# Kernel tuning notes

Hardware: AMD Instinct MI355X
Metric: run time of the kernel (lower is better)

The kernel has to match this reference:

```python
import jax, jax.numpy as jnp
import numpy as np
from jax import lax

V, D, P, C = 151936, 1024, 64, 28
B, S = 1, 1024
EPS = 1.1920929e-07  # torch.finfo(float32).eps, used by nn.RMSNorm(eps=None)


def setup_inputs() -> dict:
    key = jax.random.key(0)
    ks = jax.random.split(key, 10)
    return {
        "tokens": jax.random.randint(ks[0], (B, S), 0, V),
        "embed_table": jax.random.normal(ks[1], (V, D), jnp.float32) * 0.02,
        "plane_proj_w": jax.random.normal(ks[2], (C, 2 * P, D), jnp.float32) * (1.0 / np.sqrt(D)),
        "back_proj_w": jax.random.normal(ks[3], (C, D, 2 * P), jnp.float32) * 0.02,
        "base_angles": jax.random.normal(ks[4], (C, P), jnp.float32) * 0.1,
        "angle_gen_w": jax.random.normal(ks[5], (P, D), jnp.float32) * 0.01,
        "scales": jnp.ones((C, D), jnp.float32),
        "shifts": jnp.zeros((C, D), jnp.float32),
        "norm_w": jnp.ones((C, D), jnp.float32),
        "decay_param": jnp.float32(0.9),
        "gate_w": jax.random.normal(ks[6], (D, D), jnp.float32) * 0.02,
        "out_norm_w": jnp.ones((D,), jnp.float32),
        "lm_head_w": jax.random.normal(ks[7], (V, D), jnp.float32) * 0.02,
    }


def _rms_norm(v, w):
    return v * lax.rsqrt(jnp.mean(v * v, axis=-1, keepdims=True) + EPS) * w


def _causal_mix(x, decay_param, gate_w):
    # state_t = d*state_{t-1} + (1-d)*x_t, causal EMA over sequence
    d = jax.nn.sigmoid(decay_param)
    def step(s, xt):
        s = d * s + (1.0 - d) * xt
        return s, s
    _, ys = lax.scan(step, jnp.zeros(x.shape[::2], x.dtype)[0:0].sum(0) + jnp.zeros((x.shape[0], x.shape[2]), x.dtype), jnp.swapaxes(x, 0, 1))
    causal = jnp.swapaxes(ys, 0, 1)  # [B,S,D]
    return x + causal @ gate_w.T


def reference(tokens, embed_table, plane_proj_w, back_proj_w, base_angles,
              angle_gen_w, scales, shifts, norm_w, decay_param, gate_w,
              out_norm_w, lm_head_w):
    x = embed_table[tokens].astype(jnp.float32)  # [B,S,D]
    n_cycles = scales.shape[0]
    for i in range(n_cycles):
        # input-dependent angle offset (detached in the original)
        extra = x.mean(axis=1) @ angle_gen_w.T          # [B,P]
        angles = base_angles[i] + lax.stop_gradient(extra.mean(axis=0)) * 0.1
        if i % 4 == 0:
            x = _causal_mix(x, decay_param, gate_w)
        # learned-plane rotation
        proj = x @ plane_proj_w[i].T                     # [B,S,2P]
        n = proj.shape[-1] // 2
        a, b = proj[..., :n], proj[..., n:]
        ca, sa = jnp.cos(angles), jnp.sin(angles)
        rot = jnp.concatenate([a * ca - b * sa, a * sa + b * ca], axis=-1)
        x_rot = x + rot @ back_proj_w[i].T
        x_act = jax.nn.silu(x_rot * scales[i] + shifts[i])
        x = x + _rms_norm(x_act - x, norm_w[i])
    x = _rms_norm(x, out_norm_w)
    return x @ lm_head_w.T  # [B,S,V]
```

## Files before the change

### kernel.cpp

```cpp
#include <hip/hip_runtime.h>

typedef __attribute__((ext_vector_type(4))) float f32x4;
typedef __attribute__((ext_vector_type(8))) short bf16x8;
typedef unsigned short u16;
typedef unsigned int u32;
typedef __attribute__((ext_vector_type(4))) unsigned short u16x4;

#define EPS 1.1920929e-07f
#define S 1024
#define D 1024
#define NV 151936
#define NCYC 28
#define SMEM_BYTES 49152

__device__ __forceinline__ u16 f2bf(float f) {
  u32 u = __float_as_uint(f);
  return (u16)((u + 0x7fffu + ((u >> 16) & 1u)) >> 16);
}
__device__ __forceinline__ float bf2f(u16 h) {
  return __uint_as_float((u32)h << 16);
}
struct bfpair { u16 h, l; };
__device__ __forceinline__ bfpair split_bf(float v) {
  bfpair r;
  r.h = f2bf(v);
  r.l = f2bf(v - bf2f(r.h));
  return r;
}

__device__ __forceinline__ void gl16(const void* g, void* s) {
  __builtin_amdgcn_global_load_lds((const __attribute__((address_space(1))) u32*)g,
                                   (__attribute__((address_space(3))) u32*)s, 16, 0, 0);
}

__device__ __forceinline__ float block_sum256(float v, float* sbuf) {
  #pragma unroll
  for (int off = 32; off; off >>= 1) v += __shfl_down(v, off);
  int lane = threadIdx.x & 63, w = threadIdx.x >> 6;
  __syncthreads();
  if (lane == 0) sbuf[w] = v;
  __syncthreads();
  return sbuf[0] + sbuf[1] + sbuf[2] + sbuf[3];
}

__device__ void cvt2_range(const float* __restrict__ src, u16* __restrict__ dh,
                           u16* __restrict__ dl, size_t n4, int blkbase, int nblk) {
  for (size_t i = (size_t)(blockIdx.x - blkbase) * 256 + threadIdx.x; i < n4;
       i += (size_t)nblk * 256) {
    f32x4 v = ((const f32x4*)src)[i];
    u16x4 oh, ol;
    #pragma unroll
    for (int e = 0; e < 4; ++e) { bfpair p = split_bf(v[e]); oh[e] = p.h; ol[e] = p.l; }
    ((u16x4*)dh)[i] = oh;
    ((u16x4*)dl)[i] = ol;
  }
}

__device__ void side_cvt(const float* __restrict__ src, u16* __restrict__ dst,
                         int chunk, int blkbase) {
  const size_t n4 = (size_t)NV * D / 4;
  const size_t per = (n4 + (size_t)(NCYC * 3) - 1) / (size_t)(NCYC * 3);
  size_t lo = (size_t)chunk * per;
  size_t hi = lo + per;
  if (hi > n4) hi = n4;
  const size_t nb = (size_t)(gridDim.x - blkbase);
  for (size_t i = lo + (size_t)(blockIdx.x - blkbase) * 256 + threadIdx.x; i < hi;
       i += nb * 256) {
    f32x4 v = ((const f32x4*)src)[i];
    u16x4 o;
    #pragma unroll
    for (int e = 0; e < 4; ++e) o[e] = f2bf(v[e]);
    ((u16x4*)dst)[i] = o;
  }
}


__device__ void gather_phase(const int* tokens, const float* embed,
                             float* x, u16* xh, u16* xl, float* cp) {
  const int t = threadIdx.x;
  f32x4 creg = 0.f;
  for (int rr = 0; rr < 4; ++rr) {
    int s = blockIdx.x * 4 + rr;
    int tok = tokens[s];
    f32x4 v = ((const f32x4*)(embed + (size_t)tok * D))[t];
    u16x4 oh, ol;
    #pragma unroll
    for (int e = 0; e < 4; ++e) { bfpair p = split_bf(v[e]); oh[e] = p.h; ol[e] = p.l; }
    ((f32x4*)(x + (size_t)s * D))[t] = v;
    ((u16x4*)(xh + (size_t)s * D))[t] = oh;
    ((u16x4*)(xl + (size_t)s * D))[t] = ol;
    creg += v;
  }
  *(f32x4*)(cp + (size_t)blockIdx.x * D + t * 4) = creg;
}

template <bool CADD>
__device__ void gemm64_dbuf(char* smem, const u16* Ah_, const u16* Al_,
                            const u16* Bh_, const u16* Bl_, int K,
                            float* xout, u16* xho, u16* xlo, float* Cout) {
  const int t = threadIdx.x;
  u16* Ash = (u16*)smem;
  u16* Asl = Ash + 8192;
  u16* Bsh = Asl + 8192;
  u16* Bsl = Bsh + 8192;
  const int wave = t >> 6, lane = t & 63;
  const int fr = lane & 15, kb = lane >> 4;
  const int sr = t >> 3, skc = (t & 7) << 3;
  const int sswz = skc ^ ((sr & 7) << 3);
  const int m0 = (blockIdx.x >> 4) * 64, n0 = (blockIdx.x & 15) * 64;
  f32x4 acc[4];
  #pragma unroll
  for (int j = 0; j < 4; ++j) acc[j] = 0.f;

  auto stage = [&](int buf, int k0) {
    #pragma unroll
    for (int it = 0; it < 2; ++it) {
      int r = it * 32 + sr;
      size_t ga = (size_t)(m0 + r) * K + k0 + sswz;
      size_t gb = (size_t)(n0 + r) * K + k0 + sswz;
      int so = buf * 4096 + r * 64 + skc;
      gl16(Ah_ + ga, Ash + so);
      gl16(Al_ + ga, Asl + so);
      gl16(Bh_ + gb, Bsh + so);
      gl16(Bl_ + gb, Bsl + so);
    }
  };
  const int nt = K >> 6;
  stage(0, 0);
  __syncthreads();
  for (int kt = 0; kt < nt; ++kt) {
    const int cur = kt & 1;
    if (kt + 1 < nt) stage(cur ^ 1, (kt + 1) << 6);
    const int co = cur * 4096;
    #pragma unroll
    for (int ks = 0; ks < 2; ++ks) {
      const int cphys = (ks * 32 + kb * 8) ^ ((fr & 7) << 3);
      int oa = co + (wave * 16 + fr) * 64 + cphys;
      bf16x8 ah = *(const bf16x8*)&Ash[oa];
      bf16x8 al = *(const bf16x8*)&Asl[oa];
      #pragma unroll
      for (int j = 0; j < 4; ++j) {
        int ob = co + (j * 16 + fr) * 64 + cphys;
        bf16x8 bh = *(const bf16x8*)&Bsh[ob];
        bf16x8 bl = *(const bf16x8*)&Bsl[ob];
        acc[j] = __builtin_amdgcn_mfma_f32_16x16x32_bf16(ah, bh, acc[j], 0, 0, 0);
        acc[j] = __builtin_amdgcn_mfma_f32_16x16x32_bf16(ah, bl, acc[j], 0, 0, 0);
        acc[j] = __builtin_amdgcn_mfma_f32_16x16x32_bf16(al, bh, acc[j], 0, 0, 0);
      }
    }
    __syncthreads();
  }
  #pragma unroll
  for (int j = 0; j < 4; ++j)
    #pragma unroll
    for (int rg = 0; rg < 4; ++rg) {
      int m = m0 + wave * 16 + kb * 4 + rg;
      int n = n0 + j * 16 + fr;
      if (CADD) {
        float v = xout[(size_t)m * D + n] + acc[j][rg];
        xout[(size_t)m * D + n] = v;
        bfpair p = split_bf(v);
        xho[(size_t)m * D + n] = p.h;
        xlo[(size_t)m * D + n] = p.l;
      } else {
        Cout[(size_t)m * D + n] = acc[j][rg];
      }
    }
}

__device__ void causal_phase(char* smem, const float* x, u16* Rh, u16* Rl,
                             float dec, int G) {
  const int t = threadIdx.x;
  for (int tile = blockIdx.x; tile < 256; tile += G) {
    int s0 = (tile >> 4) * 64, d0 = (tile & 15) * 64;
    float (*tl)[64] = (float(*)[64])smem;
    for (int idx = t; idx < 159 * 64; idx += 256) {
      int rr = idx >> 6, c = idx & 63;
      int gs = s0 - 95 + rr;
      tl[rr][c] = (gs >= 0) ? x[(size_t)gs * D + d0 + c] : 0.f;
    }
    __syncthreads();
    int c = t & 63, r0 = t >> 6;
    for (int rr = r0; rr < 64; rr += 4) {
      float acc = 0.f, w = 1.f - dec;
      int base = rr + 95;
      #pragma unroll 8
      for (int j = 0; j < 96; ++j) { acc += w * tl[base - j][c]; w *= dec; }
      bfpair p = split_bf(acc);
      Rh[(size_t)(s0 + rr) * D + d0 + c] = p.h;
      Rl[(size_t)(s0 + rr) * D + d0 + c] = p.l;
    }
    __syncthreads();
  }
}

__device__ void proj_phase(char* smem, const u16* xh, const u16* xl,
                           const u16* Bh_, const u16* Bl_, float* pacc) {
  const int t = threadIdx.x;
  const int mt = blockIdx.x & 15, kq = blockIdx.x >> 4;
  const int m0 = mt * 64;
  const int k0 = kq * 64;
  u16* Ash = (u16*)smem;
  u16* Asl = Ash + 4096;
  u16* Bsh = Asl + 4096;
  u16* Bsl = Bsh + 8192;
  const int wave = t >> 6, lane = t & 63;
  const int fr = lane & 15, kb = lane >> 4;
  const int sr = t >> 3, skc = (t & 7) << 3;
  const int sswz = skc ^ ((sr & 7) << 3);
  f32x4 acc[8];
  #pragma unroll
  for (int j = 0; j < 8; ++j) acc[j] = 0.f;

  #pragma unroll
  for (int it = 0; it < 2; ++it) {
    int r = it * 32 + sr;
    size_t ga = (size_t)(m0 + r) * D + k0 + sswz;
    gl16(xh + ga, Ash + r * 64 + skc);
    gl16(xl + ga, Asl + r * 64 + skc);
  }
  #pragma unroll
  for (int it = 0; it < 4; ++it) {
    int r = it * 32 + sr;
    size_t gb = (size_t)r * D + k0 + sswz;
    gl16(Bh_ + gb, Bsh + r * 64 + skc);
    gl16(Bl_ + gb, Bsl + r * 64 + skc);
  }
  __syncthreads();
  #pragma unroll
  for (int ks = 0; ks < 2; ++ks) {
    const int cphys = (ks * 32 + kb * 8) ^ ((fr & 7) << 3);
    int oa = (wave * 16 + fr) * 64 + cphys;
    bf16x8 ah = *(const bf16x8*)&Ash[oa];
    bf16x8 al = *(const bf16x8*)&Asl[oa];
    #pragma unroll
    for (int j = 0; j < 8; ++j) {
      int ob = (j * 16 + fr) * 64 + cphys;
      bf16x8 bh = *(const bf16x8*)&Bsh[ob];
      bf16x8 bl = *(const bf16x8*)&Bsl[ob];
      acc[j] = __builtin_amdgcn_mfma_f32_16x16x32_bf16(ah, bh, acc[j], 0, 0, 0);
      acc[j] = __builtin_amdgcn_mfma_f32_16x16x32_bf16(ah, bl, acc[j], 0, 0, 0);
      acc[j] = __builtin_amdgcn_mfma_f32_16x16x32_bf16(al, bh, acc[j], 0, 0, 0);
    }
  }
  float* pb = pacc + (size_t)blockIdx.x * 64 * 128;
  #pragma unroll
  for (int j = 0; j < 8; ++j)
    #pragma unroll
    for (int rg = 0; rg < 4; ++rg) {
      int ml = wave * 16 + kb * 4 + rg;
      pb[ml * 128 + j * 16 + fr] = acc[j][rg];
    }
}

__device__ void angles_all(float* colsum, const float* cp, const float* agw,
                           const float* bang_i, float* trig) {
  const int t = threadIdx.x;
  f32x4 acc = 0.f;
  for (int b = 0; b < 256; ++b)
    acc += *(const f32x4*)(cp + (size_t)b * D + t * 4);
  *(f32x4*)&colsum[t * 4] = acc;
  __syncthreads();
  const int wave = t >> 6, lane = t & 63;
  for (int pp = 0; pp < 16; ++pp) {
    int p = wave * 16 + pp;
    float sum = 0.f;
    #pragma unroll
    for (int q = 0; q < 16; ++q) {
      int d = lane + q * 64;
      sum += colsum[d] * agw[p * D + d];
    }
    #pragma unroll
    for (int off = 32; off; off >>= 1) sum += __shfl_down(sum, off);
    if (lane == 0) {
      float ang = bang_i[p] + 0.1f * (sum * (1.f / (float)S));
      trig[p] = cosf(ang);
      trig[64 + p] = sinf(ang);
    }
  }
}

__device__ void epilogue_phase(float* sbuf, float* x, u16* xh, u16* xl,
                               const float* Rf, const float* scale,
                               const float* shift, const float* nw, float* cp) {
  const int t = threadIdx.x;
  f32x4 sc = *(const f32x4*)(scale + t * 4);
  f32x4 sh = *(const f32x4*)(shift + t * 4);
  f32x4 nwv = *(const f32x4*)(nw + t * 4);
  f32x4 creg = 0.f;
  for (int rr = 0; rr < 4; ++rr) {
    int s = blockIdx.x * 4 + rr;
    f32x4 xv = *(const f32x4*)(x + (size_t)s * D + t * 4);
    f32x4 rv = *(const f32x4*)(Rf + (size_t)s * D + t * 4);
    float y[4], ss = 0.f;
    #pragma unroll
    for (int c = 0; c < 4; ++c) {
      float xr = xv[c] + rv[c];
      float tt = xr * sc[c] + sh[c];
      float act = tt / (1.f + expf(-tt));
      y[c] = act - xv[c];
      ss += y[c] * y[c];
    }
    float total = block_sum256(ss, sbuf);
    float inv = rsqrtf(total * (1.f / (float)D) + EPS);
    f32x4 o;
    u16x4 oh, ol;
    #pragma unroll
    for (int c = 0; c < 4; ++c) {
      o[c] = xv[c] + y[c] * inv * nwv[c];
      bfpair p = split_bf(o[c]);
      oh[c] = p.h;
      ol[c] = p.l;
      creg[c] += o[c];
    }
    *(f32x4*)(x + (size_t)s * D + t * 4) = o;
    *(u16x4*)(xh + (size_t)s * D + t * 4) = oh;
    *(u16x4*)(xl + (size_t)s * D + t * 4) = ol;
  }
  *(f32x4*)(cp + (size_t)blockIdx.x * D + t * 4) = creg;
}

__device__ void outnorm_phase(float* sbuf, const float* x, const float* w, u16* xn) {
  const int t = threadIdx.x;
  for (int rr = 0; rr < 4; ++rr) {
    int s = blockIdx.x * 4 + rr;
    f32x4 xv = *(const f32x4*)(x + (size_t)s * D + t * 4);
    float total = block_sum256(xv[0]*xv[0] + xv[1]*xv[1] + xv[2]*xv[2] + xv[3]*xv[3], sbuf);
    float inv = rsqrtf(total * (1.f / (float)D) + EPS);
    f32x4 wv = *(const f32x4*)(w + t * 4);
    u16x4 o;
    #pragma unroll
    for (int c = 0; c < 4; ++c) o[c] = f2bf(xv[c] * inv * wv[c]);
    *(u16x4*)(xn + (size_t)s * D + t * 4) = o;
  }
}

__global__ __launch_bounds__(256) void fb_gather(const int* tokens, const float* embed,
                                                 float* x, u16* xh, u16* xl, float* cp,
                                                 const float* gatew, u16* gh, u16* gl,
                                                 const float* Wp, u16* Wph, u16* Wpl,
                                                 const float* Wb, u16* Wbh, u16* Wbl) {
  if (blockIdx.x < 256) {
    gather_phase(tokens, embed, x, xh, xl, cp);
  } else if (blockIdx.x < 384) {
    cvt2_range(gatew, gh, gl, (size_t)D * D / 4, 256, 128);
  } else if (blockIdx.x < 576) {
    cvt2_range(Wp, Wph, Wpl, (size_t)NCYC * 128 * D / 4, 384, 192);
  } else {
    cvt2_range(Wb, Wbh, Wbl, (size_t)NCYC * 128 * D / 4, 576, 192);
  }
}
__global__ __launch_bounds__(256) void fb_causal(const float* x, u16* Rh, u16* Rl,
                                                 const float* decay) {
  __shared__ __align__(16) char sm[40704];
  causal_phase(sm, x, Rh, Rl, 1.f / (1.f + expf(-decay[0])), gridDim.x);
}
__global__ __launch_bounds__(256) void fb_gate(const u16* Rh, const u16* Rl,
                                               const u16* gh, const u16* gl,
                                               float* x, u16* xh, u16* xl) {
  __shared__ __align__(16) char sm[65536];
  gemm64_dbuf<true>(sm, Rh, Rl, gh, gl, 1024, x, xh, xl, nullptr);
}
__global__ __launch_bounds__(256) void fb_proj(const u16* xh, const u16* xl,
                                               const u16* Wph, const u16* Wpl,
                                               const float* cp, const float* agw,
                                               const float* bang_i,
                                               float* pacc, float* trig,
                                               const float* lmw, u16* lm_bf, int chunk) {
  __shared__ __align__(16) char sm[SMEM_BYTES];
  if (blockIdx.x < 256) proj_phase(sm, xh, xl, Wph, Wpl, pacc);
  else if (blockIdx.x == 256) angles_all((float*)sm, cp, agw, bang_i, trig);
  else side_cvt(lmw, lm_bf, chunk, 257);
}

__global__ __launch_bounds__(256) void fb_back(const float* __restrict__ pacc,
                                               const float* __restrict__ trig,
                                               const u16* __restrict__ Bh_,
                                               const u16* __restrict__ Bl_,
                                               float* __restrict__ Rf,
                                               const float* lmw, u16* lm_bf, int chunk) {
  __shared__ u16 Ash[64 * 128];
  __shared__ u16 Asl[64 * 128];
  __shared__ u16 Bsh[64 * 64];
  __shared__ u16 Bsl[64 * 64];
  if (blockIdx.x >= 256) { side_cvt(lmw, lm_bf, chunk, 256); return; }
  const int t = threadIdx.x;
  const int tile = blockIdx.x;
  const int mt = tile >> 4;
  const int m0 = mt * 64, n0 = (tile & 15) * 64;
  const int wave = t >> 6, lane = t & 63;
  const int fr = lane & 15, kb = lane >> 4;
  const int sr = t >> 3, skc = (t & 7) << 3;
  const int sswz = skc ^ ((sr & 7) << 3);

  #pragma unroll
  for (int ri = 0; ri < 2; ++ri) {
    int r = ri * 32 + sr;
    int pdst = skc ^ ((r & 7) << 3);
    f32x4 a0 = 0.f, a1 = 0.f, b0 = 0.f, b1 = 0.f;
    #pragma unroll
    for (int kq = 0; kq < 16; ++kq) {
      const float* pk = pacc + ((size_t)(kq * 16 + mt) * 64 + r) * 128;
      a0 += *(const f32x4*)(pk + skc);
      a1 += *(const f32x4*)(pk + skc + 4);
      b0 += *(const f32x4*)(pk + 64 + skc);
      b1 += *(const f32x4*)(pk + 64 + skc + 4);
    }
    #pragma unroll
    for (int kh = 0; kh < 2; ++kh) {
      u16 hbuf[8], lbuf[8];
      #pragma unroll
      for (int j = 0; j < 8; ++j) {
        float av = (j < 4) ? a0[j & 3] : a1[j & 3];
        float bv = (j < 4) ? b0[j & 3] : b1[j & 3];
        float ca = trig[skc + j], sa = trig[64 + skc + j];
        float v = (kh == 0) ? (av * ca - bv * sa) : (av * sa + bv * ca);
        bfpair p = split_bf(v);
        hbuf[j] = p.h;
        lbuf[j] = p.l;
      }
      int so = r * 128 + kh * 64 + pdst;
      *(bf16x8*)&Ash[so] = *(bf16x8*)hbuf;
      *(bf16x8*)&Asl[so] = *(bf16x8*)lbuf;
    }
  }
  __syncthreads();

  f32x4 acc[4];
  #pragma unroll
  for (int j = 0; j < 4; ++j) acc[j] = 0.f;

  for (int kt = 0; kt < 2; ++kt) {
    int k0 = kt * 64;
    #pragma unroll
    for (int it = 0; it < 2; ++it) {
      int r = it * 32 + sr;
      size_t gb = (size_t)(n0 + r) * 128 + k0 + sswz;
      gl16(Bh_ + gb, Bsh + r * 64 + skc);
      gl16(Bl_ + gb, Bsl + r * 64 + skc);
    }
    __syncthreads();
    #pragma unroll
    for (int ks = 0; ks < 2; ++ks) {
      const int w = (ks * 32 + kb * 8) ^ ((fr & 7) << 3);
      int oa = (wave * 16 + fr) * 128 + k0 + w;
      bf16x8 ah = *(const bf16x8*)&Ash[oa];
      bf16x8 al = *(const bf16x8*)&Asl[oa];
      #pragma unroll
      for (int j = 0; j < 4; ++j) {
        int ob = (j * 16 + fr) * 64 + w;
        bf16x8 bh = *(const bf16x8*)&Bsh[ob];
        bf16x8 bl = *(const bf16x8*)&Bsl[ob];
        acc[j] = __builtin_amdgcn_mfma_f32_16x16x32_bf16(ah, bh, acc[j], 0, 0, 0);
        acc[j] = __builtin_amdgcn_mfma_f32_16x16x32_bf16(ah, bl, acc[j], 0, 0, 0);
        acc[j] = __builtin_amdgcn_mfma_f32_16x16x32_bf16(al, bh, acc[j], 0, 0, 0);
      }
    }
    __syncthreads();
  }
  #pragma unroll
  for (int j = 0; j < 4; ++j)
    #pragma unroll
    for (int rg = 0; rg < 4; ++rg) {
      int m = m0 + wave * 16 + kb * 4 + rg;
      int n = n0 + j * 16 + fr;
      Rf[(size_t)m * D + n] = acc[j][rg];
    }
}

__global__ __launch_bounds__(256) void fb_epi(float* x, u16* xh, u16* xl, const float* Rf,
                                              const float* scale, const float* shift,
                                              const float* nw, float* cp,
                                              const float* lmw, u16* lm_bf, int chunk) {
  __shared__ float sbuf[4];
  if (blockIdx.x < 256) epilogue_phase(sbuf, x, xh, xl, Rf, scale, shift, nw, cp);
  else side_cvt(lmw, lm_bf, chunk, 256);
}
__global__ __launch_bounds__(256) void fb_outnorm(const float* x, const float* w, u16* xn) {
  __shared__ float sbuf[4];
  outnorm_phase(sbuf, x, w, xn);
}

template <bool PRECONV>
__global__ __launch_bounds__(256) void k_lm(const u16* __restrict__ A,
                                            const void* __restrict__ Wsrc,
                                            float* __restrict__ out) {
  __shared__ u16 As[128 * 64];
  __shared__ u16 Bs[128 * 64];
  const int bid = blockIdx.x;
  const int lid = (bid & 7) * 1187 + (bid >> 3);
  const int m0 = (lid & 7) * 128;
  const int n0 = (lid >> 3) * 128;
  const int t = threadIdx.x;
  const int wave = t >> 6, lane = t & 63;
  const int wm = (wave >> 1) * 64, wn = (wave & 1) * 64;
  const int fr = lane & 15, kb = lane >> 4;
  const int sr = t >> 3, skc = (t & 7) << 3;
  const int sswz = skc ^ ((sr & 7) << 3);
  const u16* Wb16 = (const u16*)Wsrc;
  const float* Wf = (const float*)Wsrc;
  f32x4 acc[4][4];
  #pragma unroll
  for (int i = 0; i < 4; ++i)
    #pragma unroll
    for (int j = 0; j < 4; ++j) acc[i][j] = 0.f;

  for (int k0 = 0; k0 < D; k0 += 64) {
    #pragma unroll
    for (int it = 0; it < 4; ++it) {
      int r = it * 32 + sr;
      gl16(A + (size_t)(m0 + r) * D + k0 + sswz, As + r * 64 + skc);
    }
    if (PRECONV) {
      #pragma unroll
      for (int it = 0; it < 4; ++it) {
        int r = it * 32 + sr;
        gl16(Wb16 + (size_t)(n0 + r) * D + k0 + sswz, Bs + r * 64 + skc);
      }
    } else {
      #pragma unroll
      for (int it = 0; it < 4; ++it) {
        int r = it * 32 + sr;
        const float* src = Wf + (size_t)(n0 + r) * D + k0 + sswz;
        f32x4 v0 = *(const f32x4*)src;
        f32x4 v1 = *(const f32x4*)(src + 4);
        u16 h[8];
        #pragma unroll
        for (int e = 0; e < 4; ++e) { h[e] = f2bf(v0[e]); h[e + 4] = f2bf(v1[e]); }
        *(bf16x8*)&Bs[r * 64 + skc] = *(bf16x8*)h;
      }
    }
    __syncthreads();
    #pragma unroll
    for (int ks = 0; ks < 2; ++ks) {
      const int cphys = (ks * 32 + kb * 8) ^ ((fr & 7) << 3);
      bf16x8 a[4], b[4];
      #pragma unroll
      for (int i = 0; i < 4; ++i) a[i] = *(const bf16x8*)&As[(wm + i * 16 + fr) * 64 + cphys];
      #pragma unroll
      for (int j = 0; j < 4; ++j) b[j] = *(const bf16x8*)&Bs[(wn + j * 16 + fr) * 64 + cphys];
      #pragma unroll
      for (int i = 0; i < 4; ++i)
        #pragma unroll
        for (int j = 0; j < 4; ++j)
          acc[i][j] = __builtin_amdgcn_mfma_f32_16x16x32_bf16(a[i], b[j], acc[i][j], 0, 0, 0);
    }
    __syncthreads();
  }
  #pragma unroll
  for (int i = 0; i < 4; ++i)
    #pragma unroll
    for (int j = 0; j < 4; ++j)
      #pragma unroll
      for (int rg = 0; rg < 4; ++rg) {
        int m = m0 + wm + i * 16 + kb * 4 + rg;
        int n = n0 + wn + j * 16 + fr;
        out[(size_t)m * NV + n] = acc[i][j][rg];
      }
}

extern "C" void kernel_launch(void* const* d_in, const int* in_sizes, int n_in,
                              void* d_out, int out_size, void* d_ws, size_t ws_size,
                              hipStream_t stream) {
  const int* tokens = (const int*)d_in[0];
  const float* embed = (const float*)d_in[1];
  const float* Wp = (const float*)d_in[2];
  const float* Wb = (const float*)d_in[3];
  const float* bang = (const float*)d_in[4];
  const float* agw = (const float*)d_in[5];
  const float* scales = (const float*)d_in[6];
  const float* shifts = (const float*)d_in[7];
  const float* normw = (const float*)d_in[8];
  const float* decay = (const float*)d_in[9];
  const float* gatew = (const float*)d_in[10];
  const float* onorm = (const float*)d_in[11];
  const float* lmw = (const float*)d_in[12];
  float* out = (float*)d_out;

  char* ws = (char*)d_ws;
  const size_t MB = 1u << 20;
  float* x = (float*)ws;
  u16* xh = (u16*)(ws + 4 * MB);
  u16* xl = (u16*)(ws + 6 * MB);
  float* Rf = (float*)(ws + 8 * MB);
  u16* Rh = (u16*)(ws + 12 * MB);
  u16* Rl = (u16*)(ws + 14 * MB);
  float* trig = (float*)(ws + 16 * MB);
  float* cp = (float*)(ws + 17 * MB);
  u16* xn = (u16*)(ws + 20 * MB);
  u16* gate_h = (u16*)(ws + 22 * MB);
  u16* gate_l = (u16*)(ws + 24 * MB);
  u16* Wp_h = (u16*)(ws + 26 * MB);
  u16* Wp_l = (u16*)(ws + 33 * MB);
  u16* Wb_h = (u16*)(ws + 40 * MB);
  u16* Wb_l = (u16*)(ws + 47 * MB);
  float* pacc = (float*)(ws + 54 * MB);
  u16* lm_bf = (u16*)(ws + 62 * MB);

  const size_t lm_elems = (size_t)NV * D;
  bool preconv = ws_size >= 62 * MB + lm_elems * 2;
  const float* side_src = preconv ? lmw : nullptr;
  u16* side_dst = preconv ? lm_bf : nullptr;
  const int gproj = preconv ? 385 : 257;
  const int gside = preconv ? 384 : 256;

  fb_gather<<<768, 256, 0, stream>>>(tokens, embed, x, xh, xl, cp,
                                     gatew, gate_h, gate_l,
                                     Wp, Wp_h, Wp_l, Wb, Wb_h, Wb_l);
  for (int i = 0; i < NCYC; ++i) {
    const u16* Wph = Wp_h + (size_t)i * 128 * D;
    const u16* Wpl = Wp_l + (size_t)i * 128 * D;
    const u16* Wbh = Wb_h + (size_t)i * 128 * D;
    const u16* Wbl = Wb_l + (size_t)i * 128 * D;
    if ((i & 3) == 0) {
      fb_causal<<<256, 256, 0, stream>>>(x, Rh, Rl, decay);
      fb_gate<<<256, 256, 0, stream>>>(Rh, Rl, gate_h, gate_l, x, xh, xl);
    }
    fb_proj<<<gproj, 256, 0, stream>>>(xh, xl, Wph, Wpl, cp, agw, bang + i * 64,
                                       pacc, trig, side_src, side_dst, i * 3);
    fb_back<<<gside, 256, 0, stream>>>(pacc, trig, Wbh, Wbl, Rf,
                                       side_src, side_dst, i * 3 + 1);
    fb_epi<<<gside, 256, 0, stream>>>(x, xh, xl, Rf, scales + i * D, shifts + i * D,
                                      normw + i * D, cp, side_src, side_dst, i * 3 + 2);
  }
  fb_outnorm<<<256, 256, 0, stream>>>(x, onorm, xn);

  if (preconv)
    k_lm<true><<<9496, 256, 0, stream>>>(xn, lm_bf, out);
  else
    k_lm<false><<<9496, 256, 0, stream>>>(xn, lmw, out);
}
```

Baseline: 2.769 ms.

## Fuse per-cycle projection, rotation, back-projection and norm epilogue into one kernel

New measurement: 4.817 ms. 74.0% more time.

```diff
diff --git a/kernel.cpp b/kernel.cpp
--- a/kernel.cpp
+++ b/kernel.cpp
@@ -58,8 +58,9 @@
 
 __device__ void side_cvt(const float* __restrict__ src, u16* __restrict__ dst,
                          int chunk, int blkbase) {
+  if (!src) return;
   const size_t n4 = (size_t)NV * D / 4;
-  const size_t per = (n4 + (size_t)(NCYC * 3) - 1) / (size_t)(NCYC * 3);
+  const size_t per = (n4 + (size_t)NCYC - 1) / (size_t)NCYC;
   size_t lo = (size_t)chunk * per;
   size_t hi = lo + per;
   if (hi > n4) hi = n4;
@@ -74,9 +75,8 @@
   }
 }
 
-
 __device__ void gather_phase(const int* tokens, const float* embed,
-                             float* x, u16* xh, u16* xl, float* cp) {
+                             float* x, u16* xh, u16* xl, float* sc) {
   const int t = threadIdx.x;
   f32x4 creg = 0.f;
   for (int rr = 0; rr < 4; ++rr) {
@@ -91,7 +91,10 @@
     ((u16x4*)(xl + (size_t)s * D))[t] = ol;
     creg += v;
   }
-  *(f32x4*)(cp + (size_t)blockIdx.x * D + t * 4) = creg;
+  int strip = blockIdx.x >> 4;
+  #pragma unroll
+  for (int e = 0; e < 4; ++e)
+    atomicAdd(&sc[strip * 1024 + t * 4 + e], creg[e]);
 }
 
 template <bool CADD>
@@ -194,133 +197,240 @@
   }
 }
 
-__device__ void proj_phase(char* smem, const u16* xh, const u16* xl,
-                           const u16* Bh_, const u16* Bl_, float* pacc) {
+__global__ __launch_bounds__(256) void k_mega(
+    u16* __restrict__ xh, u16* __restrict__ xl,
+    const u16* __restrict__ Wph, const u16* __restrict__ Wpl,
+    const u16* __restrict__ Wbh, const u16* __restrict__ Wbl,
+    float* __restrict__ x, float* __restrict__ sc,
+    const float* __restrict__ agw, const float* __restrict__ bang_i,
+    const float* __restrict__ scale, const float* __restrict__ shift,
+    const float* __restrict__ nw, float* __restrict__ ys,
+    const float* lmw, u16* lm_bf, int chunk) {
+  __shared__ __align__(16) char sm[SMEM_BYTES];
+  __shared__ float trig_s[128];
+  if (blockIdx.x >= 16) { side_cvt(lmw, lm_bf, chunk, 16); return; }
   const int t = threadIdx.x;
-  const int mt = blockIdx.x & 15, kq = blockIdx.x >> 4;
+  const int mt = blockIdx.x;
   const int m0 = mt * 64;
-  const int k0 = kq * 64;
-  u16* Ash = (u16*)smem;
-  u16* Asl = Ash + 4096;
-  u16* Bsh = Asl + 4096;
-  u16* Bsl = Bsh + 8192;
   const int wave = t >> 6, lane = t & 63;
   const int fr = lane & 15, kb = lane >> 4;
   const int sr = t >> 3, skc = (t & 7) << 3;
   const int sswz = skc ^ ((sr & 7) << 3);
+
+  {
+    float* csum = (float*)sm;
+    f32x4 a = 0.f;
+    #pragma unroll
+    for (int s2 = 0; s2 < 16; ++s2)
+      a += *(const f32x4*)(sc + s2 * 1024 + t * 4);
+    *(f32x4*)&csum[t * 4] = a;
+    __syncthreads();
+    for (int pp = 0; pp < 16; ++pp) {
+      int p = wave * 16 + pp;
+      float sum = 0.f;
+      #pragma unroll
+      for (int q = 0; q < 16; ++q) {
+        int d = lane + q * 64;
+        sum += csum[d] * agw[p * D + d];
+      }
+      #pragma unroll
+      for (int off = 32; off; off >>= 1) sum += __shfl_down(sum, off);
+      if (lane == 0) {
+        float ang = bang_i[p] + 0.1f * (sum * (1.f / (float)S));
+        trig_s[p] = cosf(ang);
+        trig_s[64 + p] = sinf(ang);
+      }
+    }
+    __syncthreads();
+  }
+
   f32x4 acc[8];
   #pragma unroll
   for (int j = 0; j < 8; ++j) acc[j] = 0.f;
-
-  #pragma unroll
-  for (int it = 0; it < 2; ++it) {
-    int r = it * 32 + sr;
-    size_t ga = (size_t)(m0 + r) * D + k0 + sswz;
-    gl16(xh + ga, Ash + r * 64 + skc);
-    gl16(xl + ga, Asl + r * 64 + skc);
-  }
-  #pragma unroll
-  for (int it = 0; it < 4; ++it) {
-    int r = it * 32 + sr;
-    size_t gb = (size_t)r * D + k0 + sswz;
-    gl16(Bh_ + gb, Bsh + r * 64 + skc);
-    gl16(Bl_ + gb, Bsl + r * 64 + skc);
-  }
-  __syncthreads();
-  #pragma unroll
-  for (int ks = 0; ks < 2; ++ks) {
-    const int cphys = (ks * 32 + kb * 8) ^ ((fr & 7) << 3);
-    int oa = (wave * 16 + fr) * 64 + cphys;
-    bf16x8 ah = *(const bf16x8*)&Ash[oa];
-    bf16x8 al = *(const bf16x8*)&Asl[oa];
-    #pragma unroll
-    for (int j = 0; j < 8; ++j) {
-      int ob = (j * 16 + fr) * 64 + cphys;
-      bf16x8 bh = *(const bf16x8*)&Bsh[ob];
-      bf16x8 bl = *(const bf16x8*)&Bsl[ob];
-      acc[j] = __builtin_amdgcn_mfma_f32_16x16x32_bf16(ah, bh, acc[j], 0, 0, 0);
-      acc[j] = __builtin_amdgcn_mfma_f32_16x16x32_bf16(ah, bl, acc[j], 0, 0, 0);
-      acc[j] = __builtin_amdgcn_mfma_f32_16x16x32_bf16(al, bh, acc[j], 0, 0, 0);
-    }
-  }
-  float* pb = pacc + (size_t)blockIdx.x * 64 * 128;
-  #pragma unroll
-  for (int j = 0; j < 8; ++j)
+  {
+    u16* Ash = (u16*)sm;
+    u16* Asl = Ash + 4096;
+    u16* Bsh = Asl + 4096;
+    u16* Bsl = Bsh + 8192;
+    for (int kt = 0; kt < 16; ++kt) {
+      int k0 = kt * 64;
+      #pragma unroll
+      for (int it = 0; it < 2; ++it) {
+        int r = it * 32 + sr;
+        size_t ga = (size_t)(m0 + r) * D + k0 + sswz;
+        gl16(xh + ga, Ash + r * 64 + skc);
+        gl16(xl + ga, Asl + r * 64 + skc);
+      }
+      #pragma unroll
+      for (int it = 0; it < 4; ++it) {
+        int r = it * 32 + sr;
+        size_t gb = (size_t)r * D + k0 + sswz;
+        gl16(Wph + gb, Bsh + r * 64 + skc);
+        gl16(Wpl + gb, Bsl + r * 64 + skc);
+      }
+      __syncthreads();
+      #pragma unroll
+      for (int ks = 0; ks < 2; ++ks) {
+        const int cphys = (ks * 32 + kb * 8) ^ ((fr & 7) << 3);
+        int oa = (wave * 16 + fr) * 64 + cphys;
+        bf16x8 ah = *(const bf16x8*)&Ash[oa];
+        bf16x8 al = *(const bf16x8*)&Asl[oa];
+        #pragma unroll
+        for (int j = 0; j < 8; ++j) {
+          int ob = (j * 16 + fr) * 64 + cphys;
+          bf16x8 bh = *(const bf16x8*)&Bsh[ob];
+          bf16x8 bl = *(const bf16x8*)&Bsl[ob];
+          acc[j] = __builtin_amdgcn_mfma_f32_16x16x32_bf16(ah, bh, acc[j], 0, 0, 0);
+          acc[j] = __builtin_amdgcn_mfma_f32_16x16x32_bf16(ah, bl, acc[j], 0, 0, 0);
+          acc[j] = __builtin_amdgcn_mfma_f32_16x16x32_bf16(al, bh, acc[j], 0, 0, 0);
+        }
+      }
+      __syncthreads();
+    }
+  }
+
+  u16* Arh = (u16*)sm;
+  u16* Arl = Arh + 8192;
+  #pragma unroll
+  for (int j = 0; j < 4; ++j) {
+    int p = j * 16 + fr;
+    float ca = trig_s[p], sa = trig_s[64 + p];
     #pragma unroll
     for (int rg = 0; rg < 4; ++rg) {
-      int ml = wave * 16 + kb * 4 + rg;
-      pb[ml * 128 + j * 16 + fr] = acc[j][rg];
-    }
-}
-
-__device__ void angles_all(float* colsum, const float* cp, const float* agw,
-                           const float* bang_i, float* trig) {
-  const int t = threadIdx.x;
-  f32x4 acc = 0.f;
-  for (int b = 0; b < 256; ++b)
-    acc += *(const f32x4*)(cp + (size_t)b * D + t * 4);
-  *(f32x4*)&colsum[t * 4] = acc;
-  __syncthreads();
-  const int wave = t >> 6, lane = t & 63;
-  for (int pp = 0; pp < 16; ++pp) {
-    int p = wave * 16 + pp;
-    float sum = 0.f;
-    #pragma unroll
-    for (int q = 0; q < 16; ++q) {
-      int d = lane + q * 64;
-      sum += colsum[d] * agw[p * D + d];
-    }
-    #pragma unroll
-    for (int off = 32; off; off >>= 1) sum += __shfl_down(sum, off);
-    if (lane == 0) {
-      float ang = bang_i[p] + 0.1f * (sum * (1.f / (float)S));
-      trig[p] = cosf(ang);
-      trig[64 + p] = sinf(ang);
-    }
-  }
-}
-
-__device__ void epilogue_phase(float* sbuf, float* x, u16* xh, u16* xl,
-                               const float* Rf, const float* scale,
-                               const float* shift, const float* nw, float* cp) {
-  const int t = threadIdx.x;
-  f32x4 sc = *(const f32x4*)(scale + t * 4);
-  f32x4 sh = *(const f32x4*)(shift + t * 4);
-  f32x4 nwv = *(const f32x4*)(nw + t * 4);
-  f32x4 creg = 0.f;
-  for (int rr = 0; rr < 4; ++rr) {
-    int s = blockIdx.x * 4 + rr;
-    f32x4 xv = *(const f32x4*)(x + (size_t)s * D + t * 4);
-    f32x4 rv = *(const f32x4*)(Rf + (size_t)s * D + t * 4);
-    float y[4], ss = 0.f;
-    #pragma unroll
-    for (int c = 0; c < 4; ++c) {
-      float xr = xv[c] + rv[c];
-      float tt = xr * sc[c] + sh[c];
-      float act = tt / (1.f + expf(-tt));
-      y[c] = act - xv[c];
-      ss += y[c] * y[c];
-    }
-    float total = block_sum256(ss, sbuf);
-    float inv = rsqrtf(total * (1.f / (float)D) + EPS);
-    f32x4 o;
-    u16x4 oh, ol;
-    #pragma unroll
-    for (int c = 0; c < 4; ++c) {
-      o[c] = xv[c] + y[c] * inv * nwv[c];
-      bfpair p = split_bf(o[c]);
-      oh[c] = p.h;
-      ol[c] = p.l;
-      creg[c] += o[c];
-    }
-    *(f32x4*)(x + (size_t)s * D + t * 4) = o;
-    *(u16x4*)(xh + (size_t)s * D + t * 4) = oh;
-    *(u16x4*)(xl + (size_t)s * D + t * 4) = ol;
-  }
-  *(f32x4*)(cp + (size_t)blockIdx.x * D + t * 4) = creg;
-}
-
-__device__ void outnorm_phase(float* sbuf, const float* x, const float* w, u16* xn) {
+      int r = wave * 16 + kb * 4 + rg;
+      float av = acc[j][rg], bv = acc[j + 4][rg];
+      bfpair pa = split_bf(av * ca - bv * sa);
+      bfpair pb = split_bf(av * sa + bv * ca);
+      int ib = ((p & 56) ^ ((r & 7) << 3)) + (p & 7);
+      int a1 = r * 128 + ib;
+      int a2 = r * 128 + 64 + ib;
+      Arh[a1] = pa.h; Arl[a1] = pa.l;
+      Arh[a2] = pb.h; Arl[a2] = pb.l;
+    }
+  }
+  __syncthreads();
+
+  u16* Bsh3 = (u16*)(sm + 32768);
+  u16* Bsl3 = Bsh3 + 4096;
+  float ss[4] = {0.f, 0.f, 0.f, 0.f};
+  for (int nt = 0; nt < 16; ++nt) {
+    int n0 = nt * 64;
+    f32x4 acc2[4];
+    #pragma unroll
+    for (int j = 0; j < 4; ++j) acc2[j] = 0.f;
+    for (int kt = 0; kt < 2; ++kt) {
+      int k0 = kt * 64;
+      #pragma unroll
+      for (int it = 0; it < 2; ++it) {
+        int r = it * 32 + sr;
+        size_t gb = (size_t)(n0 + r) * 128 + k0 + sswz;
+        gl16(Wbh + gb, Bsh3 + r * 64 + skc);
+        gl16(Wbl + gb, Bsl3 + r * 64 + skc);
+      }
+      __syncthreads();
+      #pragma unroll
+      for (int ks = 0; ks < 2; ++ks) {
+        const int w = (ks * 32 + kb * 8) ^ ((fr & 7) << 3);
+        int oa = (wave * 16 + fr) * 128 + k0 + w;
+        bf16x8 ah = *(const bf16x8*)&Arh[oa];
+        bf16x8 al = *(const bf16x8*)&Arl[oa];
+        #pragma unroll
+        for (int j = 0; j < 4; ++j) {
+          int ob = (j * 16 + fr) * 64 + w;
+          bf16x8 bh = *(const bf16x8*)&Bsh3[ob];
+          bf16x8 bl = *(const bf16x8*)&Bsl3[ob];
+          acc2[j] = __builtin_amdgcn_mfma_f32_16x16x32_bf16(ah, bh, acc2[j], 0, 0, 0);
+          acc2[j] = __builtin_amdgcn_mfma_f32_16x16x32_bf16(ah, bl, acc2[j], 0, 0, 0);
+          acc2[j] = __builtin_amdgcn_mfma_f32_16x16x32_bf16(al, bh, acc2[j], 0, 0, 0);
+        }
+      }
+      __syncthreads();
+    }
+    #pragma unroll
+    for (int j = 0; j < 4; ++j) {
+      int n = n0 + j * 16 + fr;
+      float scv = scale[n], shv = shift[n];
+      #pragma unroll
+      for (int rg = 0; rg < 4; ++rg) {
+        int m = wave * 16 + kb * 4 + rg;
+        size_t gi = (size_t)(m0 + m) * D + n;
+        float xv = x[gi];
+        float xr = xv + acc2[j][rg];
+        float tt = xr * scv + shv;
+        float act = tt / (1.f + expf(-tt));
+        float y = act - xv;
+        ss[rg] += y * y;
+        ys[gi] = y;
+      }
+    }
+  }
+
+  #pragma unroll
+  for (int off = 1; off < 16; off <<= 1) {
+    #pragma unroll
+    for (int rg = 0; rg < 4; ++rg) ss[rg] += __shfl_xor(ss[rg], off);
+  }
+  float inv_[4];
+  #pragma unroll
+  for (int rg = 0; rg < 4; ++rg)
+    inv_[rg] = rsqrtf(ss[rg] * (1.f / (float)D) + EPS);
+
+  float* scb = (float*)sm;
+  __syncthreads();
+  *(f32x4*)&scb[t * 4] = f32x4(0.f);
+  __syncthreads();
+  for (int nt = 0; nt < 16; ++nt) {
+    #pragma unroll
+    for (int j = 0; j < 4; ++j) {
+      int n = nt * 64 + j * 16 + fr;
+      float nwv = nw[n];
+      float osum = 0.f;
+      #pragma unroll
+      for (int rg = 0; rg < 4; ++rg) {
+        int m = wave * 16 + kb * 4 + rg;
+        size_t gi = (size_t)(m0 + m) * D + n;
+        float o = x[gi] + ys[gi] * inv_[rg] * nwv;
+        x[gi] = o;
+        bfpair p = split_bf(o);
+        xh[gi] = p.h;
+        xl[gi] = p.l;
+        osum += o;
+      }
+      atomicAdd(&scb[n], osum);
+    }
+  }
+  __syncthreads();
+  *(f32x4*)(sc + mt * 1024 + t * 4) = *(const f32x4*)&scb[t * 4];
+}
+
+__global__ __launch_bounds__(256) void fb_gather(const int* tokens, const float* embed,
+                                                 float* x, u16* xh, u16* xl, float* sc,
+                                                 const float* gatew, u16* gh, u16* gl,
+                                                 const float* Wp, u16* Wph, u16* Wpl,
+                                                 const float* Wb, u16* Wbh, u16* Wbl) {
+  if (blockIdx.x < 256) {
+    gather_phase(tokens, embed, x, xh, xl, sc);
+  } else if (blockIdx.x < 384) {
+    cvt2_range(gatew, gh, gl, (size_t)D * D / 4, 256, 128);
+  } else if (blockIdx.x < 576) {
+    cvt2_range(Wp, Wph, Wpl, (size_t)NCYC * 128 * D / 4, 384, 192);
+  } else {
+    cvt2_range(Wb, Wbh, Wbl, (size_t)NCYC * 128 * D / 4, 576, 192);
+  }
+}
+__global__ __launch_bounds__(256) void fb_causal(const float* x, u16* Rh, u16* Rl,
+                                                 const float* decay) {
+  __shared__ __align__(16) char smc[40704];
+  causal_phase(smc, x, Rh, Rl, 1.f / (1.f + expf(-decay[0])), gridDim.x);
+}
+__global__ __launch_bounds__(256) void fb_gate(const u16* Rh, const u16* Rl,
+                                               const u16* gh, const u16* gl,
+                                               float* x, u16* xh, u16* xl) {
+  __shared__ __align__(16) char smg[65536];
+  gemm64_dbuf<true>(smg, Rh, Rl, gh, gl, 1024, x, xh, xl, nullptr);
+}
+__global__ __launch_bounds__(256) void fb_outnorm(const float* x, const float* w, u16* xn) {
+  __shared__ float sbuf[4];
   const int t = threadIdx.x;
   for (int rr = 0; rr < 4; ++rr) {
     int s = blockIdx.x * 4 + rr;
@@ -333,152 +443,6 @@
     for (int c = 0; c < 4; ++c) o[c] = f2bf(xv[c] * inv * wv[c]);
     *(u16x4*)(xn + (size_t)s * D + t * 4) = o;
   }
-}
-
-__global__ __launch_bounds__(256) void fb_gather(const int* tokens, const float* embed,
-                                                 float* x, u16* xh, u16* xl, float* cp,
-                                                 const float* gatew, u16* gh, u16* gl,
-                                                 const float* Wp, u16* Wph, u16* Wpl,
-                                                 const float* Wb, u16* Wbh, u16* Wbl) {
-  if (blockIdx.x < 256) {
-    gather_phase(tokens, embed, x, xh, xl, cp);
-  } else if (blockIdx.x < 384) {
-    cvt2_range(gatew, gh, gl, (size_t)D * D / 4, 256, 128);
-  } else if (blockIdx.x < 576) {
-    cvt2_range(Wp, Wph, Wpl, (size_t)NCYC * 128 * D / 4, 384, 192);
-  } else {
-    cvt2_range(Wb, Wbh, Wbl, (size_t)NCYC * 128 * D / 4, 576, 192);
-  }
-}
-__global__ __launch_bounds__(256) void fb_causal(const float* x, u16* Rh, u16* Rl,
-                                                 const float* decay) {
-  __shared__ __align__(16) char sm[40704];
-  causal_phase(sm, x, Rh, Rl, 1.f / (1.f + expf(-decay[0])), gridDim.x);
-}
-__global__ __launch_bounds__(256) void fb_gate(const u16* Rh, const u16* Rl,
-                                               const u16* gh, const u16* gl,
-                                               float* x, u16* xh, u16* xl) {
-  __shared__ __align__(16) char sm[65536];
-  gemm64_dbuf<true>(sm, Rh, Rl, gh, gl, 1024, x, xh, xl, nullptr);
-}
-__global__ __launch_bounds__(256) void fb_proj(const u16* xh, const u16* xl,
-                                               const u16* Wph, const u16* Wpl,
-                                               const float* cp, const float* agw,
-                                               const float* bang_i,
-                                               float* pacc, float* trig,
-                                               const float* lmw, u16* lm_bf, int chunk) {
-  __shared__ __align__(16) char sm[SMEM_BYTES];
-  if (blockIdx.x < 256) proj_phase(sm, xh, xl, Wph, Wpl, pacc);
-  else if (blockIdx.x == 256) angles_all((float*)sm, cp, agw, bang_i, trig);
-  else side_cvt(lmw, lm_bf, chunk, 257);
-}
-
-__global__ __launch_bounds__(256) void fb_back(const float* __restrict__ pacc,
-                                               const float* __restrict__ trig,
-                                               const u16* __restrict__ Bh_,
-                                               const u16* __restrict__ Bl_,
-                                               float* __restrict__ Rf,
-                                               const float* lmw, u16* lm_bf, int chunk) {
-  __shared__ u16 Ash[64 * 128];
-  __shared__ u16 Asl[64 * 128];
-  __shared__ u16 Bsh[64 * 64];
-  __shared__ u16 Bsl[64 * 64];
-  if (blockIdx.x >= 256) { side_cvt(lmw, lm_bf, chunk, 256); return; }
-  const int t = threadIdx.x;
-  const int tile = blockIdx.x;
-  const int mt = tile >> 4;
-  const int m0 = mt * 64, n0 = (tile & 15) * 64;
-  const int wave = t >> 6, lane = t & 63;
-  const int fr = lane & 15, kb = lane >> 4;
-  const int sr = t >> 3, skc = (t & 7) << 3;
-  const int sswz = skc ^ ((sr & 7) << 3);
-
-  #pragma unroll
-  for (int ri = 0; ri < 2; ++ri) {
-    int r = ri * 32 + sr;
-    int pdst = skc ^ ((r & 7) << 3);
-    f32x4 a0 = 0.f, a1 = 0.f, b0 = 0.f, b1 = 0.f;
-    #pragma unroll
-    for (int kq = 0; kq < 16; ++kq) {
-      const float* pk = pacc + ((size_t)(kq * 16 + mt) * 64 + r) * 128;
-      a0 += *(const f32x4*)(pk + skc);
-      a1 += *(const f32x4*)(pk + skc + 4);
-      b0 += *(const f32x4*)(pk + 64 + skc);
-      b1 += *(const f32x4*)(pk + 64 + skc + 4);
-    }
-    #pragma unroll
-    for (int kh = 0; kh < 2; ++kh) {
-      u16 hbuf[8], lbuf[8];
-      #pragma unroll
-      for (int j = 0; j < 8; ++j) {
-        float av = (j < 4) ? a0[j & 3] : a1[j & 3];
-        float bv = (j < 4) ? b0[j & 3] : b1[j & 3];
-        float ca = trig[skc + j], sa = trig[64 + skc + j];
-        float v = (kh == 0) ? (av * ca - bv * sa) : (av * sa + bv * ca);
-        bfpair p = split_bf(v);
-        hbuf[j] = p.h;
-        lbuf[j] = p.l;
-      }
-      int so = r * 128 + kh * 64 + pdst;
-      *(bf16x8*)&Ash[so] = *(bf16x8*)hbuf;
-      *(bf16x8*)&Asl[so] = *(bf16x8*)lbuf;
-    }
-  }
-  __syncthreads();
-
-  f32x4 acc[4];
-  #pragma unroll
-  for (int j = 0; j < 4; ++j) acc[j] = 0.f;
-
-  for (int kt = 0; kt < 2; ++kt) {
-    int k0 = kt * 64;
-    #pragma unroll
-    for (int it = 0; it < 2; ++it) {
-      int r = it * 32 + sr;
-      size_t gb = (size_t)(n0 + r) * 128 + k0 + sswz;
-      gl16(Bh_ + gb, Bsh + r * 64 + skc);
-      gl16(Bl_ + gb, Bsl + r * 64 + skc);
-    }
-    __syncthreads();
-    #pragma unroll
-    for (int ks = 0; ks < 2; ++ks) {
-      const int w = (ks * 32 + kb * 8) ^ ((fr & 7) << 3);
-      int oa = (wave * 16 + fr) * 128 + k0 + w;
-      bf16x8 ah = *(const bf16x8*)&Ash[oa];
-      bf16x8 al = *(const bf16x8*)&Asl[oa];
-      #pragma unroll
-      for (int j = 0; j < 4; ++j) {
-        int ob = (j * 16 + fr) * 64 + w;
-        bf16x8 bh = *(const bf16x8*)&Bsh[ob];
-        bf16x8 bl = *(const bf16x8*)&Bsl[ob];
-        acc[j] = __builtin_amdgcn_mfma_f32_16x16x32_bf16(ah, bh, acc[j], 0, 0, 0);
-        acc[j] = __builtin_amdgcn_mfma_f32_16x16x32_bf16(ah, bl, acc[j], 0, 0, 0);
-        acc[j] = __builtin_amdgcn_mfma_f32_16x16x32_bf16(al, bh, acc[j], 0, 0, 0);
-      }
-    }
-    __syncthreads();
-  }
-  #pragma unroll
-  for (int j = 0; j < 4; ++j)
-    #pragma unroll
-    for (int rg = 0; rg < 4; ++rg) {
-      int m = m0 + wave * 16 + kb * 4 + rg;
-      int n = n0 + j * 16 + fr;
-      Rf[(size_t)m * D + n] = acc[j][rg];
-    }
-}
-
-__global__ __launch_bounds__(256) void fb_epi(float* x, u16* xh, u16* xl, const float* Rf,
-                                              const float* scale, const float* shift,
-                                              const float* nw, float* cp,
-                                              const float* lmw, u16* lm_bf, int chunk) {
-  __shared__ float sbuf[4];
-  if (blockIdx.x < 256) epilogue_phase(sbuf, x, xh, xl, Rf, scale, shift, nw, cp);
-  else side_cvt(lmw, lm_bf, chunk, 256);
-}
-__global__ __launch_bounds__(256) void fb_outnorm(const float* x, const float* w, u16* xn) {
-  __shared__ float sbuf[4];
-  outnorm_phase(sbuf, x, w, xn);
 }
 
 template <bool PRECONV>
@@ -582,11 +546,10 @@
   float* x = (float*)ws;
   u16* xh = (u16*)(ws + 4 * MB);
   u16* xl = (u16*)(ws + 6 * MB);
-  float* Rf = (float*)(ws + 8 * MB);
+  float* ys = (float*)(ws + 8 * MB);
   u16* Rh = (u16*)(ws + 12 * MB);
   u16* Rl = (u16*)(ws + 14 * MB);
-  float* trig = (float*)(ws + 16 * MB);
-  float* cp = (float*)(ws + 17 * MB);
+  float* sc = (float*)(ws + 16 * MB);
   u16* xn = (u16*)(ws + 20 * MB);
   u16* gate_h = (u16*)(ws + 22 * MB);
   u16* gate_l = (u16*)(ws + 24 * MB);
@@ -594,34 +557,30 @@
   u16* Wp_l = (u16*)(ws + 33 * MB);
   u16* Wb_h = (u16*)(ws + 40 * MB);
   u16* Wb_l = (u16*)(ws + 47 * MB);
-  float* pacc = (float*)(ws + 54 * MB);
-  u16* lm_bf = (u16*)(ws + 62 * MB);
+  u16* lm_bf = (u16*)(ws + 54 * MB);
 
   const size_t lm_elems = (size_t)NV * D;
-  bool preconv = ws_size >= 62 * MB + lm_elems * 2;
+  bool preconv = ws_size >= 54 * MB + lm_elems * 2;
   const float* side_src = preconv ? lmw : nullptr;
   u16* side_dst = preconv ? lm_bf : nullptr;
-  const int gproj = preconv ? 385 : 257;
-  const int gside = preconv ? 384 : 256;
-
-  fb_gather<<<768, 256, 0, stream>>>(tokens, embed, x, xh, xl, cp,
+  const int gmega = preconv ? 144 : 16;
+
+  (void)hipMemsetAsync(sc, 0, 16 * 1024 * sizeof(float), stream);
+
+  fb_gather<<<768, 256, 0, stream>>>(tokens, embed, x, xh, xl, sc,
                                      gatew, gate_h, gate_l,
                                      Wp, Wp_h, Wp_l, Wb, Wb_h, Wb_l);
   for (int i = 0; i < NCYC; ++i) {
-    const u16* Wph = Wp_h + (size_t)i * 128 * D;
-    const u16* Wpl = Wp_l + (size_t)i * 128 * D;
-    const u16* Wbh = Wb_h + (size_t)i * 128 * D;
-    const u16* Wbl = Wb_l + (size_t)i * 128 * D;
     if ((i & 3) == 0) {
       fb_causal<<<256, 256, 0, stream>>>(x, Rh, Rl, decay);
       fb_gate<<<256, 256, 0, stream>>>(Rh, Rl, gate_h, gate_l, x, xh, xl);
     }
-    fb_proj<<<gproj, 256, 0, stream>>>(xh, xl, Wph, Wpl, cp, agw, bang + i * 64,
-                                       pacc, trig, side_src, side_dst, i * 3);
-    fb_back<<<gside, 256, 0, stream>>>(pacc, trig, Wbh, Wbl, Rf,
-                                       side_src, side_dst, i * 3 + 1);
-    fb_epi<<<gside, 256, 0, stream>>>(x, xh, xl, Rf, scales + i * D, shifts + i * D,
-                                      normw + i * D, cp, side_src, side_dst, i * 3 + 2);
+    k_mega<<<gmega, 256, 0, stream>>>(xh, xl,
+                                      Wp_h + (size_t)i * 128 * D, Wp_l + (size_t)i * 128 * D,
+                                      Wb_h + (size_t)i * 128 * D, Wb_l + (size_t)i * 128 * D,
+                                      x, sc, agw, bang + i * 64,
+                                      scales + i * D, shifts + i * D, normw + i * D,
+                                      ys, side_src, side_dst, i);
   }
   fb_outnorm<<<256, 256, 0, stream>>>(x, onorm, xn);
 
```
